# Kernel optimization log

Measured on AMD Instinct MI355X. Metric: run time of the kernel, lower is better.

The kernel has to match this reference:

```python
import jax, jax.numpy as jnp
import numpy as np

SIZE = 512
WIDTH_TILES = 1
N_STROKES = 16
STROKE_WIDTH = 0.04
N_SAMPLES = 32


def setup_inputs() -> dict:
    key = jax.random.key(0)
    # matches torch.rand(n_free,4,2)*0.6+0.2 init
    control_points = jax.random.uniform(key, (N_STROKES, 4, 2), dtype=jnp.float32) * 0.6 + 0.2
    ys = jnp.linspace(0.0, 1.0, SIZE)
    xs = jnp.linspace(0.0, 1.0, SIZE * WIDTH_TILES)
    grid_y, grid_x = jnp.meshgrid(ys, xs, indexing='ij')
    pixel_grid = jnp.stack([grid_x, grid_y], axis=-1).reshape(-1, 2).astype(jnp.float32)  # [HW,2]
    return {"control_points": control_points, "pixel_grid": pixel_grid}


def _bezier3_samples(curves):
    # curves: [S,4,2] -> [S,N_SAMPLES,2]
    ts = jnp.linspace(0.0, 1.0, N_SAMPLES, dtype=curves.dtype)
    t = ts[None, :, None]
    mt = 1.0 - t
    p0, p1, p2, p3 = (curves[:, k:k + 1, :] for k in range(4))
    return mt ** 3 * p0 + 3 * mt ** 2 * t * p1 + 3 * mt * t ** 2 * p2 + t ** 3 * p3


def reference(control_points, pixel_grid):
    pts = jnp.clip(control_points, 0.0, 1.0)  # all_strokes(), symmetric=False, no groups
    pts_flat = _bezier3_samples(pts).reshape(-1, 2)  # [P,2], P = S*N_SAMPLES
    sharpness = float(N_SAMPLES) * 8.0
    # pairwise pixel-to-sample distances: [HW,P]
    diff = pixel_grid[:, None, :] - pts_flat[None, :, :]
    dist = jnp.sqrt(jnp.sum(diff * diff, axis=-1))
    # softmin via logsumexp
    min_dist = -jax.scipy.special.logsumexp(-sharpness * dist, axis=-1) / sharpness  # [HW]
    coverage = jax.nn.sigmoid((STROKE_WIDTH - min_dist) * (8.0 / STROKE_WIDTH))
    return (1.0 - coverage).reshape(SIZE, SIZE * WIDTH_TILES)[None]  # (1,H,W)
```

## Files before the change

### kernel.cpp

```cpp
#include <hip/hip_runtime.h>


#define SIZE    512
#define NPAIRS  256
#define NGRP    128
#define MARGIN  0.05f
#define LOG2E   1.4426950408889634f
#define C2      (256.0f * LOG2E)
#define FART2   0.009025f

typedef float v2f __attribute__((ext_vector_type(2)));
typedef float v4f __attribute__((ext_vector_type(4)));

__device__ __forceinline__ float sqrt_raw(float x) { return __builtin_amdgcn_sqrtf(x); }
__device__ __forceinline__ float exp2_raw(float x) { return __builtin_amdgcn_exp2f(x); }
__device__ __forceinline__ float log2_raw(float x) { return __builtin_amdgcn_logf(x); }
__device__ __forceinline__ float rcp_raw(float x)  { return __builtin_amdgcn_rcpf(x); }
__device__ __forceinline__ float clamp01(float x)  { return fminf(fmaxf(x, 0.0f), 1.0f); }

__global__ __launch_bounds__(256) void bezier_glyph_kernel(
    const float* __restrict__ cp,
    const float* __restrict__ grid,
    float* __restrict__ out)
{
    __shared__ v4f sxy[NPAIRS];
    __shared__ v2f sp2[NPAIRS];
    __shared__ v4f sbox[NGRP];
    __shared__ v4f srep[NGRP];

    const int tid = threadIdx.x;

    {
        float px[2], py[2], pq[2];
#pragma unroll
        for (int k = 0; k < 2; ++k) {
            const int i = 2 * tid + k;
            const int stroke = i >> 5, samp = i & 31;
            const float t  = (float)samp * (1.0f / 31.0f);
            const float mt = 1.0f - t;
            const float b0 = mt * mt * mt;
            const float b1 = 3.0f * mt * mt * t;
            const float b2 = 3.0f * mt * t * t;
            const float b3 = t * t * t;
            const float* p = cp + stroke * 8;
            px[k] = b0 * clamp01(p[0]) + b1 * clamp01(p[2]) + b2 * clamp01(p[4]) + b3 * clamp01(p[6]);
            py[k] = b0 * clamp01(p[1]) + b1 * clamp01(p[3]) + b2 * clamp01(p[5]) + b3 * clamp01(p[7]);
            pq[k] = px[k] * px[k] + py[k] * py[k];
        }
        sxy[tid] = (v4f){px[0], px[1], py[0], py[1]};
        sp2[tid] = (v2f){pq[0], pq[1]};
    }
    __syncthreads();

    if (tid < NGRP) {
        const v4f a0 = sxy[2 * tid];
        const v4f a1 = sxy[2 * tid + 1];
        const float lox = fminf(fminf(a0.x, a0.y), fminf(a1.x, a1.y));
        const float hix = fmaxf(fmaxf(a0.x, a0.y), fmaxf(a1.x, a1.y));
        const float loy = fminf(fminf(a0.z, a0.w), fminf(a1.z, a1.w));
        const float hiy = fmaxf(fmaxf(a0.z, a0.w), fmaxf(a1.z, a1.w));
        sbox[tid] = (v4f){lox, loy, hix, hiy};
        srep[tid] = (v4f){a0.y, a0.w, a1.x, a1.z};
    }
    __syncthreads();

    const int lane = tid & 63;
    const int wv   = tid >> 6;
    const int rect = ((wv << 10 | blockIdx.x) * 2897) & 4095;
    const int px0 = (rect & 63) << 3;
    const int py0 = (rect >> 6) << 3;
    const int x = px0 + (lane & 7);
    const int y = py0 + (lane >> 3);

    const float inv511 = 1.0f / 511.0f;
    const float rx0 = (float)px0 * inv511, rx1 = (float)(px0 + 7) * inv511;
    const float ry0 = (float)py0 * inv511, ry1 = (float)(py0 + 7) * inv511;
    const float cxr = 0.5f * (rx0 + rx1);
    const float cyr = 0.5f * (ry0 + ry1);
    const float hd  = 0.009686f;

    const v4f b0 = sbox[lane];
    const v4f b1 = sbox[lane + 64];
    const float bdx0 = fmaxf(fmaxf(b0.x - rx1, rx0 - b0.z), 0.0f);
    const float bdy0 = fmaxf(fmaxf(b0.y - ry1, ry0 - b0.w), 0.0f);
    const float db2_0 = bdx0 * bdx0 + bdy0 * bdy0;
    const float bdx1 = fmaxf(fmaxf(b1.x - rx1, rx0 - b1.z), 0.0f);
    const float bdy1 = fmaxf(fmaxf(b1.y - ry1, ry0 - b1.w), 0.0f);
    const float db2_1 = bdx1 * bdx1 + bdy1 * bdy1;

    float mdb = fminf(db2_0, db2_1);
#pragma unroll
    for (int s = 1; s < 64; s <<= 1) mdb = fminf(mdb, __shfl_xor(mdb, s));
    if (mdb > FART2) {
        out[y * SIZE + x] = 1.0f;
        return;
    }

    const v4f r0 = srep[lane];
    const v4f r1 = srep[lane + 64];
    float dr;
    {
        const float e0x = cxr - r0.x, e0y = cyr - r0.y;
        const float e1x = cxr - r0.z, e1y = cyr - r0.w;
        const float e2x = cxr - r1.x, e2y = cyr - r1.y;
        const float e3x = cxr - r1.z, e3y = cyr - r1.w;
        dr = fminf(fminf(e0x * e0x + e0y * e0y, e1x * e1x + e1y * e1y),
                   fminf(e2x * e2x + e2y * e2y, e3x * e3x + e3y * e3y));
    }
    float dc = sqrt_raw(dr);
#pragma unroll
    for (int s = 1; s < 64; s <<= 1) dc = fminf(dc, __shfl_xor(dc, s));
    const float ub  = dc + hd;
    const float tau = ub + MARGIN;
    const float tau2 = tau * tau;
    const unsigned long long mask_lo = __ballot(db2_0 < tau2);
    const unsigned long long mask_hi = __ballot(db2_1 < tau2);

    const float2 g = reinterpret_cast<const float2*>(grid)[y * SIZE + x];
    const float n2gx = -2.0f * g.x;
    const float n2gy = -2.0f * g.y;
    const float g2   = g.x * g.x + g.y * g.y;
    const v2f   g2v  = {g2, g2};
    const float bias = C2 * ub;

    float s0 = 0.0f, s1 = 0.0f;
#pragma unroll
    for (int h = 0; h < 2; ++h) {
        unsigned long long mm = h ? mask_hi : mask_lo;
        const int goff = h << 6;
        while (mm) {
            const int gi = __ffsll(mm) - 1;
            mm &= mm - 1;
            const int base = (goff + gi) << 1;
#pragma unroll
            for (int k = 0; k < 2; ++k) {
                const v4f a = sxy[base + k];
                const v2f q = sp2[base + k];
                const v2f u = (v2f){a.x, a.y} * n2gx + ((v2f){a.z, a.w} * n2gy + q);
                const v2f d2v = u + g2v;
                const float da = sqrt_raw(fmaxf(d2v.x, 0.0f));
                const float db = sqrt_raw(fmaxf(d2v.y, 0.0f));
                s0 += exp2_raw(__builtin_fmaf(-C2, da, bias));
                s1 += exp2_raw(__builtin_fmaf(-C2, db, bias));
            }
        }
    }
    const float s = s0 + s1;

    const float min_dist = ub - log2_raw(s) * (1.0f / C2);
    const float z  = (0.04f - min_dist) * 200.0f;
    const float ez = exp2_raw(z * LOG2E);
    out[y * SIZE + x] = rcp_raw(1.0f + ez);
}

extern "C" void kernel_launch(void* const* d_in, const int* in_sizes, int n_in,
                              void* d_out, int out_size, void* d_ws, size_t ws_size,
                              hipStream_t stream) {
    const float* cp   = (const float*)d_in[0];
    const float* grid = (const float*)d_in[1];
    float* out = (float*)d_out;

    bezier_glyph_kernel<<<1024, 256, 0, stream>>>(cp, grid, out);
}
```

Baseline: 62.44 us.

## Split each pixel's sample groups across two lanes and combine with a shuffle

Measured after the change: 61.68 us. Within noise of the previous version (-1.2%).

```diff
diff --git a/kernel.cpp b/kernel.cpp
--- a/kernel.cpp
+++ b/kernel.cpp
@@ -4,10 +4,12 @@
 #define SIZE    512
 #define NPAIRS  256
 #define NGRP    128
+#define BLOCK   512
 #define MARGIN  0.05f
 #define LOG2E   1.4426950408889634f
 #define C2      (256.0f * LOG2E)
 #define FART2   0.009025f
+#define EVENM   0x5555555555555555ull
 
 typedef float v2f __attribute__((ext_vector_type(2)));
 typedef float v4f __attribute__((ext_vector_type(4)));
@@ -18,7 +20,7 @@
 __device__ __forceinline__ float rcp_raw(float x)  { return __builtin_amdgcn_rcpf(x); }
 __device__ __forceinline__ float clamp01(float x)  { return fminf(fmaxf(x, 0.0f), 1.0f); }
 
-__global__ __launch_bounds__(256) void bezier_glyph_kernel(
+__global__ __launch_bounds__(BLOCK) void bezier_glyph_kernel(
     const float* __restrict__ cp,
     const float* __restrict__ grid,
     float* __restrict__ out)
@@ -30,7 +32,7 @@
 
     const int tid = threadIdx.x;
 
-    {
+    if (tid < NPAIRS) {
         float px[2], py[2], pq[2];
 #pragma unroll
         for (int k = 0; k < 2; ++k) {
@@ -64,20 +66,22 @@
     }
     __syncthreads();
 
-    const int lane = tid & 63;
-    const int wv   = tid >> 6;
-    const int rect = ((wv << 10 | blockIdx.x) * 2897) & 4095;
+    const int lane   = tid & 63;
+    const int parity = lane & 1;
+    const int k      = lane >> 1;
+    const int wid    = (blockIdx.x << 3) | (tid >> 6);
+    const int rect   = (wid * 2897) & 8191;
     const int px0 = (rect & 63) << 3;
-    const int py0 = (rect >> 6) << 3;
-    const int x = px0 + (lane & 7);
-    const int y = py0 + (lane >> 3);
+    const int py0 = (rect >> 6) << 2;
+    const int x = px0 + (k & 7);
+    const int y = py0 + (k >> 3);
 
     const float inv511 = 1.0f / 511.0f;
     const float rx0 = (float)px0 * inv511, rx1 = (float)(px0 + 7) * inv511;
-    const float ry0 = (float)py0 * inv511, ry1 = (float)(py0 + 7) * inv511;
+    const float ry0 = (float)py0 * inv511, ry1 = (float)(py0 + 3) * inv511;
     const float cxr = 0.5f * (rx0 + rx1);
     const float cyr = 0.5f * (ry0 + ry1);
-    const float hd  = 0.009686f;
+    const float hd  = 0.007452f;
 
     const v4f b0 = sbox[lane];
     const v4f b1 = sbox[lane + 64];
@@ -92,7 +96,7 @@
 #pragma unroll
     for (int s = 1; s < 64; s <<= 1) mdb = fminf(mdb, __shfl_xor(mdb, s));
     if (mdb > FART2) {
-        out[y * SIZE + x] = 1.0f;
+        if (parity == 0) out[y * SIZE + x] = 1.0f;
         return;
     }
 
@@ -113,8 +117,9 @@
     const float ub  = dc + hd;
     const float tau = ub + MARGIN;
     const float tau2 = tau * tau;
-    const unsigned long long mask_lo = __ballot(db2_0 < tau2);
-    const unsigned long long mask_hi = __ballot(db2_1 < tau2);
+    const unsigned long long pm = parity ? ~EVENM : EVENM;
+    const unsigned long long mask_lo = __ballot(db2_0 < tau2) & pm;
+    const unsigned long long mask_hi = __ballot(db2_1 < tau2) & pm;
 
     const float2 g = reinterpret_cast<const float2*>(grid)[y * SIZE + x];
     const float n2gx = -2.0f * g.x;
@@ -133,9 +138,9 @@
             mm &= mm - 1;
             const int base = (goff + gi) << 1;
 #pragma unroll
-            for (int k = 0; k < 2; ++k) {
-                const v4f a = sxy[base + k];
-                const v2f q = sp2[base + k];
+            for (int kk = 0; kk < 2; ++kk) {
+                const v4f a = sxy[base + kk];
+                const v2f q = sp2[base + kk];
                 const v2f u = (v2f){a.x, a.y} * n2gx + ((v2f){a.z, a.w} * n2gy + q);
                 const v2f d2v = u + g2v;
                 const float da = sqrt_raw(fmaxf(d2v.x, 0.0f));
@@ -145,12 +150,13 @@
             }
         }
     }
-    const float s = s0 + s1;
+    float s = s0 + s1;
+    s += __shfl_xor(s, 1);
 
     const float min_dist = ub - log2_raw(s) * (1.0f / C2);
     const float z  = (0.04f - min_dist) * 200.0f;
     const float ez = exp2_raw(z * LOG2E);
-    out[y * SIZE + x] = rcp_raw(1.0f + ez);
+    if (parity == 0) out[y * SIZE + x] = rcp_raw(1.0f + ez);
 }
 
 extern "C" void kernel_launch(void* const* d_in, const int* in_sizes, int n_in,
@@ -160,5 +166,5 @@
     const float* grid = (const float*)d_in[1];
     float* out = (float*)d_out;
 
-    bezier_glyph_kernel<<<1024, 256, 0, stream>>>(cp, grid, out);
+    bezier_glyph_kernel<<<1024, BLOCK, 0, stream>>>(cp, grid, out);
 }
```
